# Kernel optimization log

Hardware: AMD Instinct MI355X
Metric: run time of the kernel (lower is better)

Reference implementation:

```python
import jax, jax.numpy as jnp
import numpy as np

N, E, H, MID = 4096, 384, 6, 96  # n_refs, embed_dim, num_heads, mlp mid dim (max(E//4,32))
DH = E // H  # head dim = 64


def setup_inputs() -> dict:
    key = jax.random.key(0)
    ks = jax.random.split(key, 12)
    def w(k, shape, fan_in):
        return jax.random.normal(k, shape, jnp.float32) / np.float32(np.sqrt(fan_in))
    return {
        "low": jax.random.normal(ks[0], (N, E), jnp.float32),
        "high": jax.random.normal(ks[1], (N, E), jnp.float32),
        "ref_w": jax.random.uniform(ks[2], (N,), jnp.float32) + 0.1,
        "low_w1": w(ks[3], (E, MID), E), "low_b1": jnp.zeros((MID,), jnp.float32),
        "low_w2": w(ks[4], (MID, E), MID), "low_b2": jnp.zeros((E,), jnp.float32),
        "high_w1": w(ks[5], (E, MID), E), "high_b1": jnp.zeros((MID,), jnp.float32),
        "high_w2": w(ks[6], (MID, E), MID), "high_b2": jnp.zeros((E,), jnp.float32),
        "layer_fuse": jnp.array([0.4, 0.6], jnp.float32),
        "wqkv": w(ks[7], (E, 3 * E), E), "bqkv": jnp.zeros((3 * E,), jnp.float32),
        "wo": w(ks[8], (E, E), E), "bo": jnp.zeros((E,), jnp.float32),
        "ln_g": jnp.ones((E,), jnp.float32), "ln_b": jnp.zeros((E,), jnp.float32),
    }


def _channel_mlp(x, w1, b1, w2, b2):
    h = jax.nn.gelu(x @ w1 + b1, approximate=False)  # [N, MID]
    return x * jax.nn.sigmoid(h @ w2 + b2)           # [N, E]


def _forward(low, high, ref_w, low_w1, low_b1, low_w2, low_b2,
             high_w1, high_b1, high_w2, high_b2, layer_fuse,
             wqkv, bqkv, wo, bo, ln_g, ln_b):
    lw = jax.nn.softmax(layer_fuse)
    fused = lw[0] * _channel_mlp(low, low_w1, low_b1, low_w2, low_b2) \
          + lw[1] * _channel_mlp(high, high_w1, high_b1, high_w2, high_b2)  # [N, E]
    # single-layer MHA over the n-reference sequence (batch of 1, batch_first)
    qkv = fused @ wqkv + bqkv                      # [N, 3E]
    q, k, v = jnp.split(qkv, 3, axis=-1)
    q = q.reshape(N, H, DH).transpose(1, 0, 2)     # [H, N, DH]
    k = k.reshape(N, H, DH).transpose(1, 0, 2)
    v = v.reshape(N, H, DH).transpose(1, 0, 2)
    scores = jnp.einsum("hnd,hmd->hnm", q, k) / np.float32(np.sqrt(DH))
    attn = jax.nn.softmax(scores, axis=-1)         # [H, N, N]
    ctx = jnp.einsum("hnm,hmd->hnd", attn, v)      # [H, N, DH]
    attn_out = ctx.transpose(1, 0, 2).reshape(N, E) @ wo + bo
    x = attn_out + fused                           # residual
    mu = jnp.mean(x, axis=-1, keepdims=True)
    var = jnp.mean(jnp.square(x - mu), axis=-1, keepdims=True)
    x = (x - mu) / jnp.sqrt(var + 1e-5) * ln_g + ln_b
    w = ref_w / jnp.sum(ref_w)
    res = jnp.sum(x * w[:, None], axis=0)          # weighted mean over refs -> [E]
    return res / (jnp.linalg.norm(res) + 1e-8)


def reference(low, high, ref_w, low_w1, low_b1, low_w2, low_b2,
              high_w1, high_b1, high_w2, high_b2, layer_fuse,
              wqkv, bqkv, wo, bo, ln_g, ln_b):
    return _forward(low, high, ref_w, low_w1, low_b1, low_w2, low_b2,
                    high_w1, high_b1, high_w2, high_b2, layer_fuse,
                    wqkv, bqkv, wo, bo, ln_g, ln_b)
```

## Files before the change

### kernel.cpp

```cpp
#include <hip/hip_runtime.h>
#include <math.h>

#define Nn 4096
#define Ee 384
#define Hh 6
#define DHh 64
#define MIDm 96
#define TEe 1152
#define SPLIT 8

typedef short s16x8 __attribute__((ext_vector_type(8)));
typedef float f32x4 __attribute__((ext_vector_type(4)));
typedef float f32x16 __attribute__((ext_vector_type(16)));
typedef unsigned short ushort_t;
typedef unsigned short ushort4_t __attribute__((ext_vector_type(4)));

#define CROW(r, hf) ((((r) & 3)) + 8 * ((r) >> 2) + 4 * (hf))

__device__ __forceinline__ float gelu_exact(float x) {
    return 0.5f * x * (1.0f + erff(x * 0.70710678118654752f));
}
__device__ __forceinline__ float sigmoidf_(float x) {
    return 1.0f / (1.0f + __expf(-x));
}
__device__ __forceinline__ ushort_t f2bf(float x) {
    unsigned int u = __float_as_uint(x);
    u = (u + 0x7FFFu + ((u >> 16) & 1u)) >> 16;
    return (ushort_t)u;
}
__device__ __forceinline__ float bf2f(ushort_t u) {
    return __uint_as_float(((unsigned int)u) << 16);
}
__device__ __forceinline__ unsigned int cvtpk(float a, float b) {
    unsigned int r;
    asm("v_cvt_pk_bf16_f32 %0, %1, %2" : "=v"(r) : "v"(a), "v"(b));
    return r;
}
__device__ __forceinline__ void gld16(const ushort_t* g, ushort_t* l) {
    __builtin_amdgcn_global_load_lds(
        (const __attribute__((address_space(1))) unsigned int*)g,
        (__attribute__((address_space(3))) unsigned int*)l, 16, 0, 0);
}

#define W1L_OFF 0
#define W1H_OFF 36864
#define W2L_OFF 73728
#define W2H_OFF 110592
#define WQKV_OFF 147456
#define WO_OFF 589824

__global__ __launch_bounds__(256) void k_cvt(
    const float* __restrict__ lw1, const float* __restrict__ hw1,
    const float* __restrict__ lw2, const float* __restrict__ hw2,
    const float* __restrict__ wqkv, const float* __restrict__ wo,
    ushort_t* __restrict__ wT) {
    __shared__ float tl[32][33];
    const int b = blockIdx.x;
    const float* src;
    int R, C, doff, ti;
    if (b < 36)       { src = lw1;  R = 384; C = 96;   doff = W1L_OFF;  ti = b; }
    else if (b < 72)  { src = hw1;  R = 384; C = 96;   doff = W1H_OFF;  ti = b - 36; }
    else if (b < 108) { src = lw2;  R = 96;  C = 384;  doff = W2L_OFF;  ti = b - 72; }
    else if (b < 144) { src = hw2;  R = 96;  C = 384;  doff = W2H_OFF;  ti = b - 108; }
    else if (b < 576) { src = wqkv; R = 384; C = 1152; doff = WQKV_OFF; ti = b - 144; }
    else              { src = wo;   R = 384; C = 384;  doff = WO_OFF;   ti = b - 576; }
    const int tcn = C >> 5;
    const int tr = ti / tcn, tc = ti % tcn;
    const int col = threadIdx.x & 31, r8 = threadIdx.x >> 5;
#pragma unroll
    for (int i = 0; i < 4; i++) {
        const int row = r8 + 8 * i;
        tl[row][col] = src[(size_t)(tr * 32 + row) * C + tc * 32 + col];
    }
    __syncthreads();
#pragma unroll
    for (int i = 0; i < 4; i++) {
        const int rowp = r8 + 8 * i;
        wT[doff + (size_t)(tc * 32 + rowp) * R + tr * 32 + col] = f2bf(tl[col][rowp]);
    }
}

__global__ __launch_bounds__(256) void k_mlp(
    const float* __restrict__ low, const float* __restrict__ high,
    const float* __restrict__ lf, const ushort_t* __restrict__ wT,
    const float* __restrict__ lb1, const float* __restrict__ lb2,
    const float* __restrict__ hb1, const float* __restrict__ hb2,
    ushort_t* __restrict__ fusedb) {
    __shared__ ushort_t Hs[2][16][104];
    __shared__ ushort_t Sg[2][16][384];
    const int t = threadIdx.x;
    const int w = t >> 6, l = t & 63, l15 = l & 15, g4 = l >> 4;
    const int st = w >> 1, nh = w & 1;
    const int rb = blockIdx.x * 16;
    const float* Xf = st ? high : low;
    const ushort_t* w1T = wT + (st ? W1H_OFF : W1L_OFF);
    const ushort_t* w2T = wT + (st ? W2H_OFF : W2L_OFF);
    const float* b1p = st ? hb1 : lb1;
    const float* b2p = st ? hb2 : lb2;
    {
        f32x4 hA[3];
#pragma unroll
        for (int nt = 0; nt < 3; nt++) hA[nt] = (f32x4){0.f, 0.f, 0.f, 0.f};
        for (int ks = 0; ks < 12; ks++) {
            const float* ap = &Xf[(size_t)(rb + l15) * 384 + ks * 32 + g4 * 8];
            f32x4 a0 = *(const f32x4*)ap;
            f32x4 a1 = *(const f32x4*)(ap + 4);
            union { unsigned int uw[4]; s16x8 v; } ua;
            ua.uw[0] = cvtpk(a0[0], a0[1]);
            ua.uw[1] = cvtpk(a0[2], a0[3]);
            ua.uw[2] = cvtpk(a1[0], a1[1]);
            ua.uw[3] = cvtpk(a1[2], a1[3]);
#pragma unroll
            for (int nt = 0; nt < 3; nt++) {
                s16x8 bf = *(const s16x8*)&w1T[(nh * 48 + nt * 16 + l15) * 384 + ks * 32 + g4 * 8];
                hA[nt] = __builtin_amdgcn_mfma_f32_16x16x32_bf16(ua.v, bf, hA[nt], 0, 0, 0);
            }
        }
#pragma unroll
        for (int nt = 0; nt < 3; nt++) {
            const int mc = nh * 48 + nt * 16 + l15;
            const float bb = b1p[mc];
#pragma unroll
            for (int r = 0; r < 4; r++)
                Hs[st][g4 * 4 + r][mc] = f2bf(gelu_exact(hA[nt][r] + bb));
        }
    }
    __syncthreads();
    {
        f32x4 sA[12];
#pragma unroll
        for (int nt = 0; nt < 12; nt++) sA[nt] = (f32x4){0.f, 0.f, 0.f, 0.f};
#pragma unroll
        for (int ks = 0; ks < 3; ks++) {
            s16x8 af = *(const s16x8*)&Hs[st][l15][ks * 32 + g4 * 8];
#pragma unroll
            for (int nt = 0; nt < 12; nt++) {
                s16x8 bf = *(const s16x8*)&w2T[(nh * 192 + nt * 16 + l15) * 96 + ks * 32 + g4 * 8];
                sA[nt] = __builtin_amdgcn_mfma_f32_16x16x32_bf16(af, bf, sA[nt], 0, 0, 0);
            }
        }
#pragma unroll
        for (int nt = 0; nt < 12; nt++) {
            const float bb = b2p[nh * 192 + nt * 16 + l15];
#pragma unroll
            for (int r = 0; r < 4; r++)
                Sg[st][g4 * 4 + r][nh * 192 + nt * 16 + l15] = f2bf(sigmoidf_(sA[nt][r] + bb));
        }
    }
    __syncthreads();
    {
        const float a0 = lf[0], a1 = lf[1];
        const float mx = fmaxf(a0, a1);
        const float e0 = __expf(a0 - mx), e1 = __expf(a1 - mx);
        const float inv = 1.0f / (e0 + e1);
        const float w0 = e0 * inv, w1v = e1 * inv;
        for (int base = t * 4; base < 16 * 384; base += 256 * 4) {
            const int row = base / 384, e0i = base % 384;
            const int gr = rb + row;
            f32x4 lo4 = *(const f32x4*)&low[(size_t)gr * 384 + e0i];
            f32x4 hi4 = *(const f32x4*)&high[(size_t)gr * 384 + e0i];
            ushort4_t s0 = *(const ushort4_t*)&Sg[0][row][e0i];
            ushort4_t s1 = *(const ushort4_t*)&Sg[1][row][e0i];
            ushort4_t fb;
#pragma unroll
            for (int i = 0; i < 4; i++)
                fb[i] = f2bf(w0 * lo4[i] * bf2f(s0[i]) + w1v * hi4[i] * bf2f(s1[i]));
            *(ushort4_t*)&fusedb[(size_t)gr * 384 + e0i] = fb;
        }
    }
}

__global__ __launch_bounds__(128) void k_qkv(
    const ushort_t* __restrict__ fusedb, const ushort_t* __restrict__ wT,
    const float* __restrict__ bqkv,
    ushort_t* __restrict__ qb, ushort_t* __restrict__ kb, ushort_t* __restrict__ vtb) {
    __shared__ float tls[2][32][40];
    const int t = threadIdx.x;
    const int w = t >> 6, l = t & 63, ll = l & 31, hf = l >> 5;
    const int rb = blockIdx.x * 32;
    const int cb = blockIdx.y * 192 + w * 96;
    const ushort_t* wq = wT + WQKV_OFF;
    f32x16 acc[3];
#pragma unroll
    for (int nt = 0; nt < 3; nt++)
#pragma unroll
        for (int r = 0; r < 16; r++) acc[nt][r] = 0.0f;
    for (int ks = 0; ks < 24; ks++) {
        s16x8 af = *(const s16x8*)&fusedb[(size_t)(rb + ll) * 384 + ks * 16 + hf * 8];
#pragma unroll
        for (int nt = 0; nt < 3; nt++) {
            s16x8 bf = *(const s16x8*)&wq[(size_t)(cb + nt * 32 + ll) * 384 + ks * 16 + hf * 8];
            acc[nt] = __builtin_amdgcn_mfma_f32_32x32x16_bf16(af, bf, acc[nt], 0, 0, 0);
        }
    }
#pragma unroll
    for (int nt = 0; nt < 3; nt++) {
        const int nb = cb + nt * 32;
        const int which = nb / 384, wn = nb % 384;
        const int hb = wn >> 6, d0 = wn & 63;
        const float bias = bqkv[nb + ll];
        if (which == 2) {
            const int d = d0 + ll;
#pragma unroll
            for (int g2 = 0; g2 < 4; g2++) {
                ushort4_t u4;
#pragma unroll
                for (int i2 = 0; i2 < 4; i2++) u4[i2] = f2bf(acc[nt][g2 * 4 + i2] + bias);
                *(ushort4_t*)&vtb[((size_t)(hb * 64 + d)) * Nn + rb + 8 * g2 + 4 * hf] = u4;
            }
        } else {
            const float sc = (which == 0) ? 0.18033688f : 1.0f;
#pragma unroll
            for (int r = 0; r < 16; r++) tls[w][CROW(r, hf)][ll] = (acc[nt][r] + bias) * sc;
            ushort_t* dst = which ? kb : qb;
            const int row2 = l >> 1, sg = l & 1;
            union { ushort_t us[16]; s16x8 v[2]; } u;
#pragma unroll
            for (int j = 0; j < 16; j++) u.us[j] = f2bf(tls[w][row2][sg * 16 + j]);
            size_t base = ((size_t)hb * Nn + rb + row2) * 64 + d0 + sg * 16;
            *(s16x8*)&dst[base] = u.v[0];
            *(s16x8*)&dst[base + 8] = u.v[1];
        }
    }
}

__global__ __launch_bounds__(512) void k_attn(
    const ushort_t* __restrict__ qb, const ushort_t* __restrict__ kb,
    const ushort_t* __restrict__ vtb, ushort_t* __restrict__ pof,
    float* __restrict__ pml) {
    __shared__ ushort_t Kt[3][4096];
    __shared__ ushort_t Vt[3][4096];
    const int t = threadIdx.x;
    const int wid8 = t >> 6, l = t & 63, ll = l & 31, hf = l >> 5;
    const int lid = blockIdx.x;
    const int xcd = lid & 7, gi = lid >> 3;
    const int pair = xcd * 6 + (gi >> 4);
    const int qt = gi & 15;
    const int h = pair % Hh, sp = pair / Hh;
    const int qrow0 = qt * 256 + wid8 * 32;
    const int srow = t >> 3;
    const int sslot = ((l & 7) ^ (l >> 3)) * 8;
    const int wch = wid8 * 512;
    const ushort_t* kbase = kb + (size_t)h * Nn * DHh;
    const ushort_t* vbase = vtb + (size_t)h * DHh * Nn;
    const int kst0 = sp * (Nn / SPLIT);
#define NT (Nn / (64 * SPLIT))
#define STAGE(B, TI) { const int ktb2 = kst0 + (TI) * 64;                                \
        gld16(kbase + (size_t)(ktb2 + srow) * DHh + sslot, &Kt[B][wch]);                 \
        gld16(vbase + (size_t)srow * Nn + ktb2 + sslot, &Vt[B][wch]); }

    s16x8 qf[4];
#pragma unroll
    for (int dc = 0; dc < 4; dc++)
        qf[dc] = *(const s16x8*)&qb[((size_t)h * Nn + qrow0 + ll) * DHh + dc * 16 + hf * 8];
    f32x16 zro;
#pragma unroll
    for (int r = 0; r < 16; r++) zro[r] = 0.0f;
    f32x16 o0 = zro, o1 = zro;
    float lsum = 0.0f;
    const int xorl = (ll & 7) << 3;

    STAGE(0, 0);
    STAGE(1, 1);
    asm volatile("s_waitcnt vmcnt(2)" ::: "memory");
    __builtin_amdgcn_s_barrier();
    __builtin_amdgcn_sched_barrier(0);
    int cur = 0;
    for (int kt = 0; kt < NT; kt++) {
        int nb = cur + 2; if (nb >= 3) nb -= 3;
        if (kt + 2 < NT) STAGE(nb, kt + 2);
        const ushort_t* KtC = Kt[cur];
        const ushort_t* VtC = Vt[cur];
        __builtin_amdgcn_s_setprio(1);
        f32x16 s0, s1;
        {
            const int colE = hf * 8;
            s16x8 kf0 = *(const s16x8*)&KtC[ll * 64 + (colE ^ xorl)];
            s16x8 kf1 = *(const s16x8*)&KtC[(32 + ll) * 64 + (colE ^ xorl)];
            s0 = __builtin_amdgcn_mfma_f32_32x32x16_bf16(kf0, qf[0], zro, 0, 0, 0);
            s1 = __builtin_amdgcn_mfma_f32_32x32x16_bf16(kf1, qf[0], zro, 0, 0, 0);
        }
#pragma unroll
        for (int dc = 1; dc < 4; dc++) {
            const int colE = dc * 16 + hf * 8;
            s16x8 kf0 = *(const s16x8*)&KtC[ll * 64 + (colE ^ xorl)];
            s16x8 kf1 = *(const s16x8*)&KtC[(32 + ll) * 64 + (colE ^ xorl)];
            s0 = __builtin_amdgcn_mfma_f32_32x32x16_bf16(kf0, qf[dc], s0, 0, 0, 0);
            s1 = __builtin_amdgcn_mfma_f32_32x32x16_bf16(kf1, qf[dc], s1, 0, 0, 0);
        }
        __builtin_amdgcn_s_setprio(0);
#pragma unroll
        for (int r = 0; r < 16; r++) { s0[r] = exp2f(s0[r]); lsum += s0[r]; }
#pragma unroll
        for (int r = 0; r < 16; r++) { s1[r] = exp2f(s1[r]); lsum += s1[r]; }
#pragma unroll
        for (int ks = 0; ks < 4; ks++) {
            const f32x16 S = (ks < 2) ? s0 : s1;
            const int b = (ks & 1) * 8;
            unsigned int t1 = cvtpk(S[b + 0], S[b + 1]);
            unsigned int t3 = cvtpk(S[b + 2], S[b + 3]);
            unsigned int t2 = cvtpk(S[b + 4], S[b + 5]);
            unsigned int t4 = cvtpk(S[b + 6], S[b + 7]);
            asm("v_permlane32_swap_b32 %0, %1" : "+v"(t1), "+v"(t2));
            asm("v_permlane32_swap_b32 %0, %1" : "+v"(t3), "+v"(t4));
            union { unsigned int uw[4]; s16x8 v; } u;
            u.uw[0] = t1;
            u.uw[1] = t3;
            u.uw[2] = t2;
            u.uw[3] = t4;
            const int colE = ks * 16 + hf * 8;
            s16x8 vf0 = *(const s16x8*)&VtC[ll * 64 + (colE ^ xorl)];
            s16x8 vf1 = *(const s16x8*)&VtC[(32 + ll) * 64 + (colE ^ xorl)];
            o0 = __builtin_amdgcn_mfma_f32_32x32x16_bf16(vf0, u.v, o0, 0, 0, 0);
            o1 = __builtin_amdgcn_mfma_f32_32x32x16_bf16(vf1, u.v, o1, 0, 0, 0);
        }
        __builtin_amdgcn_sched_barrier(0);
        asm volatile("s_waitcnt vmcnt(2)" ::: "memory");
        __builtin_amdgcn_s_barrier();
        __builtin_amdgcn_sched_barrier(0);
        cur = cur + 1; if (cur >= 3) cur = 0;
    }
    lsum += __shfl_xor(lsum, 32, 64);
    const size_t bq = ((size_t)sp * 256 + (qrow0 >> 4) + (ll >> 4)) * 384;
    const int q15 = ll & 15;
#pragma unroll
    for (int r = 0; r < 16; r++) {
        const int e_a = h * 64 + CROW(r, hf);
        pof[(bq + e_a) * 16 + q15] = f2bf(o0[r]);
        pof[(bq + e_a + 32) * 16 + q15] = f2bf(o1[r]);
    }
    if (hf == 0)
        pml[((size_t)sp * Hh + h) * Nn + qrow0 + ll] = lsum;
#undef STAGE
#undef NT
}

__global__ __launch_bounds__(512) void k_oln(
    const ushort_t* __restrict__ pof, const float* __restrict__ pml,
    const ushort_t* __restrict__ wT, const float* __restrict__ bo,
    const ushort_t* __restrict__ fusedb,
    const float* __restrict__ lng, const float* __restrict__ lnb,
    const float* __restrict__ rw, float* __restrict__ part) {
    __shared__ ushort_t cx[16][384];
    __shared__ float xs[16][388];
    __shared__ float stats[16][2];
    __shared__ float dinvs[Hh][16];
    const int t = threadIdx.x;
    const int w = t >> 6, l = t & 63, l15 = l & 15, g4 = l >> 4;
    const int rb = blockIdx.x * 16;
    const int rbq = blockIdx.x;
    if (t < Hh * 16) {
        const int hh = t >> 4, qq = t & 15;
        float den = 0.0f;
#pragma unroll
        for (int s = 0; s < SPLIT; s++)
            den += pml[((size_t)s * Hh + hh) * Nn + rb + qq];
        dinvs[hh][qq] = 1.0f / den;
    }
    __syncthreads();
    for (int task = t; task < 768; task += 512) {
        const int e = task >> 1, half = task & 1;
        const int hh = e >> 6;
        float a8[8];
#pragma unroll
        for (int j = 0; j < 8; j++) a8[j] = 0.0f;
#pragma unroll
        for (int s = 0; s < SPLIT; s++) {
            s16x8 v = *(const s16x8*)&pof[(((size_t)s * 256 + rbq) * 384 + e) * 16 + half * 8];
#pragma unroll
            for (int j = 0; j < 8; j++) a8[j] += bf2f((ushort_t)v[j]);
        }
#pragma unroll
        for (int j = 0; j < 8; j++) {
            const int q = half * 8 + j;
            cx[q][e ^ ((q & 7) << 3)] = f2bf(a8[j] * dinvs[hh][q]);
        }
    }
    __syncthreads();
    const ushort_t* woT = wT + WO_OFF;
    f32x4 oA[3];
#pragma unroll
    for (int nt = 0; nt < 3; nt++) oA[nt] = (f32x4){0.f, 0.f, 0.f, 0.f};
    const int xo = (l15 & 7) << 3;
    for (int ks = 0; ks < 12; ks++) {
        s16x8 af = *(const s16x8*)&cx[l15][(ks * 32 + g4 * 8) ^ xo];
#pragma unroll
        for (int nt = 0; nt < 3; nt++) {
            s16x8 bf = *(const s16x8*)&woT[(size_t)(w * 48 + nt * 16 + l15) * 384 + ks * 32 + g4 * 8];
            oA[nt] = __builtin_amdgcn_mfma_f32_16x16x32_bf16(af, bf, oA[nt], 0, 0, 0);
        }
    }
#pragma unroll
    for (int nt = 0; nt < 3; nt++) {
        const int col = w * 48 + nt * 16 + l15;
        const float bias = bo[col];
#pragma unroll
        for (int r = 0; r < 4; r++) {
            const int row = g4 * 4 + r;
            xs[row][col] = oA[nt][r] + bias + bf2f(fusedb[(size_t)(rb + row) * 384 + col]);
        }
    }
    __syncthreads();
    {
        const int row = t >> 5, j = t & 31;
        float s1 = 0.0f, s2 = 0.0f;
        for (int i = 0; i < 12; i++) {
            const float x = xs[row][j + 32 * i];
            s1 += x;
            s2 += x * x;
        }
#pragma unroll
        for (int off = 1; off < 32; off <<= 1) {
            s1 += __shfl_xor(s1, off, 64);
            s2 += __shfl_xor(s2, off, 64);
        }
        if (j == 0) {
            const float mu = s1 * (1.0f / Ee);
            const float var = s2 * (1.0f / Ee) - mu * mu;
            stats[row][0] = mu;
            stats[row][1] = rsqrtf(var + 1e-5f);
        }
    }
    __syncthreads();
    for (int c = t; c < 384; c += 512) {
        const float gt = lng[c], bb = lnb[c];
        float acc = 0.0f;
        for (int r = 0; r < 16; r++) {
            const float xn = (xs[r][c] - stats[r][0]) * stats[r][1] * gt + bb;
            acc += xn * rw[rb + r];
        }
        part[(size_t)blockIdx.x * Ee + c] = acc;
    }
}

__global__ __launch_bounds__(384) void k_final(const float* __restrict__ part,
                                               const float* __restrict__ rw,
                                               float* __restrict__ outp) {
    __shared__ float red[6], redw[6];
    const int t = threadIdx.x;
    float s = 0.0f;
    for (int b = 0; b < 256; b++) s += part[(size_t)b * Ee + t];
    float wsp = 0.0f;
    for (int i = t; i < Nn; i += 384) wsp += rw[i];
    float q2 = s * s;
#pragma unroll
    for (int off = 32; off > 0; off >>= 1) {
        q2 += __shfl_down(q2, off, 64);
        wsp += __shfl_down(wsp, off, 64);
    }
    const int wid = t >> 6, lane = t & 63;
    if (lane == 0) { red[wid] = q2; redw[wid] = wsp; }
    __syncthreads();
    float tot = 0.0f, wtot = 0.0f;
#pragma unroll
    for (int w = 0; w < 6; w++) { tot += red[w]; wtot += redw[w]; }
    outp[t] = s / (sqrtf(tot) + 1e-8f * wtot);
}

extern "C" void kernel_launch(void* const* d_in, const int* in_sizes, int n_in,
                              void* d_out, int out_size, void* d_ws, size_t ws_size,
                              hipStream_t stream) {
    const float* low  = (const float*)d_in[0];
    const float* high = (const float*)d_in[1];
    const float* rw   = (const float*)d_in[2];
    const float* lw1  = (const float*)d_in[3];
    const float* lb1  = (const float*)d_in[4];
    const float* lw2  = (const float*)d_in[5];
    const float* lb2  = (const float*)d_in[6];
    const float* hw1  = (const float*)d_in[7];
    const float* hb1  = (const float*)d_in[8];
    const float* hw2  = (const float*)d_in[9];
    const float* hb2  = (const float*)d_in[10];
    const float* lf   = (const float*)d_in[11];
    const float* wqkv = (const float*)d_in[12];
    const float* bqkv = (const float*)d_in[13];
    const float* wo   = (const float*)d_in[14];
    const float* bo   = (const float*)d_in[15];
    const float* lng  = (const float*)d_in[16];
    const float* lnb  = (const float*)d_in[17];

    float* ws = (float*)d_ws;
    const size_t NE = (size_t)Nn * Ee;
    float* pml  = ws;
    float* part = ws + 196608;
    ushort_t* u16base = (ushort_t*)(ws + 294912);
    ushort_t* fusedb = u16base;
    ushort_t* vtb    = u16base + NE;
    ushort_t* qb     = u16base + 2 * NE;
    ushort_t* kb     = u16base + 3 * NE;
    ushort_t* wT     = u16base + 4 * NE;
    ushort_t* pof    = wT + 737280;

    hipLaunchKernelGGL(k_cvt, dim3(720), dim3(256), 0, stream,
                       lw1, hw1, lw2, hw2, wqkv, wo, wT);
    hipLaunchKernelGGL(k_mlp, dim3(256), dim3(256), 0, stream,
                       low, high, lf, wT, lb1, lb2, hb1, hb2, fusedb);
    hipLaunchKernelGGL(k_qkv, dim3(128, 6), dim3(128), 0, stream,
                       fusedb, wT, bqkv, qb, kb, vtb);
    hipLaunchKernelGGL(k_attn, dim3(Hh * SPLIT * 16), dim3(512), 0, stream,
                       qb, kb, vtb, pof, pml);
    hipLaunchKernelGGL(k_oln, dim3(256), dim3(512), 0, stream,
                       pof, pml, wT, bo, fusedb, lng, lnb, rw, part);
    hipLaunchKernelGGL(k_final, dim3(1), dim3(384), 0, stream, part, rw, (float*)d_out);
}
```

Baseline: 124.3 us.

## Process 64 query rows per wave in attention to reuse K/V fragments

Changes the attention kernel from 8 waves with 32 query rows each to 4 waves with 64 query rows each. Each K and V fragment read from LDS now feeds twice as many MFMAs, which halves LDS read traffic per unit of work. Each thread now issues twice as many global-to-LDS loads, and the wait counts are adjusted to match. The cost is roughly double the accumulator registers and fewer waves per block, which may lower occupancy and latency hiding.

```diff
diff --git a/kernel.cpp b/kernel.cpp
--- a/kernel.cpp
+++ b/kernel.cpp
@@ -224,45 +224,48 @@
     }
 }
 
-__global__ __launch_bounds__(512) void k_attn(
+__global__ __launch_bounds__(256) void k_attn(
     const ushort_t* __restrict__ qb, const ushort_t* __restrict__ kb,
     const ushort_t* __restrict__ vtb, ushort_t* __restrict__ pof,
     float* __restrict__ pml) {
     __shared__ ushort_t Kt[3][4096];
     __shared__ ushort_t Vt[3][4096];
     const int t = threadIdx.x;
-    const int wid8 = t >> 6, l = t & 63, ll = l & 31, hf = l >> 5;
+    const int w = t >> 6, l = t & 63, ll = l & 31, hf = l >> 5;
     const int lid = blockIdx.x;
     const int xcd = lid & 7, gi = lid >> 3;
     const int pair = xcd * 6 + (gi >> 4);
     const int qt = gi & 15;
     const int h = pair % Hh, sp = pair / Hh;
-    const int qrow0 = qt * 256 + wid8 * 32;
+    const int qrow0 = qt * 256 + w * 64;
     const int srow = t >> 3;
     const int sslot = ((l & 7) ^ (l >> 3)) * 8;
-    const int wch = wid8 * 512;
     const ushort_t* kbase = kb + (size_t)h * Nn * DHh;
     const ushort_t* vbase = vtb + (size_t)h * DHh * Nn;
     const int kst0 = sp * (Nn / SPLIT);
 #define NT (Nn / (64 * SPLIT))
 #define STAGE(B, TI) { const int ktb2 = kst0 + (TI) * 64;                                \
-        gld16(kbase + (size_t)(ktb2 + srow) * DHh + sslot, &Kt[B][wch]);                 \
-        gld16(vbase + (size_t)srow * Nn + ktb2 + sslot, &Vt[B][wch]); }
-
-    s16x8 qf[4];
-#pragma unroll
-    for (int dc = 0; dc < 4; dc++)
-        qf[dc] = *(const s16x8*)&qb[((size_t)h * Nn + qrow0 + ll) * DHh + dc * 16 + hf * 8];
+        gld16(kbase + (size_t)(ktb2 + srow) * DHh + sslot, &Kt[B][w * 512]);             \
+        gld16(kbase + (size_t)(ktb2 + srow + 32) * DHh + sslot, &Kt[B][2048 + w * 512]); \
+        gld16(vbase + (size_t)srow * Nn + ktb2 + sslot, &Vt[B][w * 512]);                \
+        gld16(vbase + (size_t)(srow + 32) * Nn + ktb2 + sslot, &Vt[B][2048 + w * 512]); }
+
+    s16x8 qf0[4], qf1[4];
+#pragma unroll
+    for (int dc = 0; dc < 4; dc++) {
+        qf0[dc] = *(const s16x8*)&qb[((size_t)h * Nn + qrow0 + ll) * DHh + dc * 16 + hf * 8];
+        qf1[dc] = *(const s16x8*)&qb[((size_t)h * Nn + qrow0 + 32 + ll) * DHh + dc * 16 + hf * 8];
+    }
     f32x16 zro;
 #pragma unroll
     for (int r = 0; r < 16; r++) zro[r] = 0.0f;
-    f32x16 o0 = zro, o1 = zro;
-    float lsum = 0.0f;
+    f32x16 o00 = zro, o01 = zro, o10 = zro, o11 = zro;
+    float lsum0 = 0.0f, lsum1 = 0.0f;
     const int xorl = (ll & 7) << 3;
 
     STAGE(0, 0);
     STAGE(1, 1);
-    asm volatile("s_waitcnt vmcnt(2)" ::: "memory");
+    asm volatile("s_waitcnt vmcnt(4)" ::: "memory");
     __builtin_amdgcn_s_barrier();
     __builtin_amdgcn_sched_barrier(0);
     int cur = 0;
@@ -272,65 +275,94 @@
         const ushort_t* KtC = Kt[cur];
         const ushort_t* VtC = Vt[cur];
         __builtin_amdgcn_s_setprio(1);
-        f32x16 s0, s1;
+        f32x16 s00, s01, s10, s11;
         {
             const int colE = hf * 8;
             s16x8 kf0 = *(const s16x8*)&KtC[ll * 64 + (colE ^ xorl)];
             s16x8 kf1 = *(const s16x8*)&KtC[(32 + ll) * 64 + (colE ^ xorl)];
-            s0 = __builtin_amdgcn_mfma_f32_32x32x16_bf16(kf0, qf[0], zro, 0, 0, 0);
-            s1 = __builtin_amdgcn_mfma_f32_32x32x16_bf16(kf1, qf[0], zro, 0, 0, 0);
+            s00 = __builtin_amdgcn_mfma_f32_32x32x16_bf16(kf0, qf0[0], zro, 0, 0, 0);
+            s10 = __builtin_amdgcn_mfma_f32_32x32x16_bf16(kf1, qf0[0], zro, 0, 0, 0);
+            s01 = __builtin_amdgcn_mfma_f32_32x32x16_bf16(kf0, qf1[0], zro, 0, 0, 0);
+            s11 = __builtin_amdgcn_mfma_f32_32x32x16_bf16(kf1, qf1[0], zro, 0, 0, 0);
         }
 #pragma unroll
         for (int dc = 1; dc < 4; dc++) {
             const int colE = dc * 16 + hf * 8;
             s16x8 kf0 = *(const s16x8*)&KtC[ll * 64 + (colE ^ xorl)];
             s16x8 kf1 = *(const s16x8*)&KtC[(32 + ll) * 64 + (colE ^ xorl)];
-            s0 = __builtin_amdgcn_mfma_f32_32x32x16_bf16(kf0, qf[dc], s0, 0, 0, 0);
-            s1 = __builtin_amdgcn_mfma_f32_32x32x16_bf16(kf1, qf[dc], s1, 0, 0, 0);
+            s00 = __builtin_amdgcn_mfma_f32_32x32x16_bf16(kf0, qf0[dc], s00, 0, 0, 0);
+            s10 = __builtin_amdgcn_mfma_f32_32x32x16_bf16(kf1, qf0[dc], s10, 0, 0, 0);
+            s01 = __builtin_amdgcn_mfma_f32_32x32x16_bf16(kf0, qf1[dc], s01, 0, 0, 0);
+            s11 = __builtin_amdgcn_mfma_f32_32x32x16_bf16(kf1, qf1[dc], s11, 0, 0, 0);
         }
         __builtin_amdgcn_s_setprio(0);
 #pragma unroll
-        for (int r = 0; r < 16; r++) { s0[r] = exp2f(s0[r]); lsum += s0[r]; }
-#pragma unroll
-        for (int r = 0; r < 16; r++) { s1[r] = exp2f(s1[r]); lsum += s1[r]; }
+        for (int r = 0; r < 16; r++) { s00[r] = exp2f(s00[r]); lsum0 += s00[r]; }
+#pragma unroll
+        for (int r = 0; r < 16; r++) { s10[r] = exp2f(s10[r]); lsum0 += s10[r]; }
+#pragma unroll
+        for (int r = 0; r < 16; r++) { s01[r] = exp2f(s01[r]); lsum1 += s01[r]; }
+#pragma unroll
+        for (int r = 0; r < 16; r++) { s11[r] = exp2f(s11[r]); lsum1 += s11[r]; }
 #pragma unroll
         for (int ks = 0; ks < 4; ks++) {
-            const f32x16 S = (ks < 2) ? s0 : s1;
+            const f32x16 SA = (ks < 2) ? s00 : s10;
+            const f32x16 SB = (ks < 2) ? s01 : s11;
             const int b = (ks & 1) * 8;
-            unsigned int t1 = cvtpk(S[b + 0], S[b + 1]);
-            unsigned int t3 = cvtpk(S[b + 2], S[b + 3]);
-            unsigned int t2 = cvtpk(S[b + 4], S[b + 5]);
-            unsigned int t4 = cvtpk(S[b + 6], S[b + 7]);
-            asm("v_permlane32_swap_b32 %0, %1" : "+v"(t1), "+v"(t2));
-            asm("v_permlane32_swap_b32 %0, %1" : "+v"(t3), "+v"(t4));
-            union { unsigned int uw[4]; s16x8 v; } u;
-            u.uw[0] = t1;
-            u.uw[1] = t3;
-            u.uw[2] = t2;
-            u.uw[3] = t4;
+            unsigned int a1 = cvtpk(SA[b + 0], SA[b + 1]);
+            unsigned int a3 = cvtpk(SA[b + 2], SA[b + 3]);
+            unsigned int a2 = cvtpk(SA[b + 4], SA[b + 5]);
+            unsigned int a4 = cvtpk(SA[b + 6], SA[b + 7]);
+            asm("v_permlane32_swap_b32 %0, %1" : "+v"(a1), "+v"(a2));
+            asm("v_permlane32_swap_b32 %0, %1" : "+v"(a3), "+v"(a4));
+            unsigned int b1 = cvtpk(SB[b + 0], SB[b + 1]);
+            unsigned int b3 = cvtpk(SB[b + 2], SB[b + 3]);
+            unsigned int b2 = cvtpk(SB[b + 4], SB[b + 5]);
+            unsigned int b4 = cvtpk(SB[b + 6], SB[b + 7]);
+            asm("v_permlane32_swap_b32 %0, %1" : "+v"(b1), "+v"(b2));
+            asm("v_permlane32_swap_b32 %0, %1" : "+v"(b3), "+v"(b4));
+            union { unsigned int uw[4]; s16x8 v; } uA, uB;
+            uA.uw[0] = a1; uA.uw[1] = a3; uA.uw[2] = a2; uA.uw[3] = a4;
+            uB.uw[0] = b1; uB.uw[1] = b3; uB.uw[2] = b2; uB.uw[3] = b4;
             const int colE = ks * 16 + hf * 8;
             s16x8 vf0 = *(const s16x8*)&VtC[ll * 64 + (colE ^ xorl)];
             s16x8 vf1 = *(const s16x8*)&VtC[(32 + ll) * 64 + (colE ^ xorl)];
-            o0 = __builtin_amdgcn_mfma_f32_32x32x16_bf16(vf0, u.v, o0, 0, 0, 0);
-            o1 = __builtin_amdgcn_mfma_f32_32x32x16_bf16(vf1, u.v, o1, 0, 0, 0);
+            o00 = __builtin_amdgcn_mfma_f32_32x32x16_bf16(vf0, uA.v, o00, 0, 0, 0);
+            o01 = __builtin_amdgcn_mfma_f32_32x32x16_bf16(vf1, uA.v, o01, 0, 0, 0);
+            o10 = __builtin_amdgcn_mfma_f32_32x32x16_bf16(vf0, uB.v, o10, 0, 0, 0);
+            o11 = __builtin_amdgcn_mfma_f32_32x32x16_bf16(vf1, uB.v, o11, 0, 0, 0);
         }
         __builtin_amdgcn_sched_barrier(0);
-        asm volatile("s_waitcnt vmcnt(2)" ::: "memory");
+        asm volatile("s_waitcnt vmcnt(4)" ::: "memory");
         __builtin_amdgcn_s_barrier();
         __builtin_amdgcn_sched_barrier(0);
         cur = cur + 1; if (cur >= 3) cur = 0;
     }
-    lsum += __shfl_xor(lsum, 32, 64);
-    const size_t bq = ((size_t)sp * 256 + (qrow0 >> 4) + (ll >> 4)) * 384;
+    lsum0 += __shfl_xor(lsum0, 32, 64);
+    lsum1 += __shfl_xor(lsum1, 32, 64);
     const int q15 = ll & 15;
-#pragma unroll
-    for (int r = 0; r < 16; r++) {
-        const int e_a = h * 64 + CROW(r, hf);
-        pof[(bq + e_a) * 16 + q15] = f2bf(o0[r]);
-        pof[(bq + e_a + 32) * 16 + q15] = f2bf(o1[r]);
-    }
-    if (hf == 0)
-        pml[((size_t)sp * Hh + h) * Nn + qrow0 + ll] = lsum;
+    {
+        const size_t bq = ((size_t)sp * 256 + (qrow0 >> 4) + (ll >> 4)) * 384;
+#pragma unroll
+        for (int r = 0; r < 16; r++) {
+            const int e_a = h * 64 + CROW(r, hf);
+            pof[(bq + e_a) * 16 + q15] = f2bf(o00[r]);
+            pof[(bq + e_a + 32) * 16 + q15] = f2bf(o01[r]);
+        }
+        if (hf == 0)
+            pml[((size_t)sp * Hh + h) * Nn + qrow0 + ll] = lsum0;
+    }
+    {
+        const size_t bq = ((size_t)sp * 256 + ((qrow0 + 32) >> 4) + (ll >> 4)) * 384;
+#pragma unroll
+        for (int r = 0; r < 16; r++) {
+            const int e_a = h * 64 + CROW(r, hf);
+            pof[(bq + e_a) * 16 + q15] = f2bf(o10[r]);
+            pof[(bq + e_a + 32) * 16 + q15] = f2bf(o11[r]);
+        }
+        if (hf == 0)
+            pml[((size_t)sp * Hh + h) * Nn + qrow0 + 32 + ll] = lsum1;
+    }
 #undef STAGE
 #undef NT
 }
@@ -497,7 +529,7 @@
                        low, high, lf, wT, lb1, lb2, hb1, hb2, fusedb);
     hipLaunchKernelGGL(k_qkv, dim3(128, 6), dim3(128), 0, stream,
                        fusedb, wT, bqkv, qb, kb, vtb);
-    hipLaunchKernelGGL(k_attn, dim3(Hh * SPLIT * 16), dim3(512), 0, stream,
+    hipLaunchKernelGGL(k_attn, dim3(Hh * SPLIT * 16), dim3(256), 0, stream,
                        qb, kb, vtb, pof, pml);
     hipLaunchKernelGGL(k_oln, dim3(256), dim3(512), 0, stream,
                        pof, pml, wT, bo, fusedb, lng, lnb, rw, part);
```

Result: slower. 132.9 us (+7.0%).
